# Optimization experiments

Measured on AMD Instinct MI355X. Metric: run time of the kernel, lower is better.

Reference implementation:

```python
import jax, jax.numpy as jnp
import numpy as np

B, U, H, M, D = 64, 1024, 16, 512, 4  # batch, units, numheads, memsize, depth
HS = U // H  # headsize


def setup_inputs() -> dict:
    key = jax.random.key(0)
    ks = jax.random.split(key, 6)
    scale = 0.02
    return {
        "x": jax.random.normal(ks[0], (B, U), jnp.float32),
        "memory": jax.random.normal(ks[1], (B, M * U), jnp.float32),
        "Wr": jax.random.normal(ks[2], (D, U, H * (M + 1)), jnp.float32) * scale,
        "br": jnp.zeros((D, H * (M + 1)), jnp.float32),
        "Ww": jax.random.normal(ks[3], (D, U, H * M), jnp.float32) * scale,
        "bw": jnp.zeros((D, H * M), jnp.float32),
        "Wk": jax.random.normal(ks[4], (D, U, U), jnp.float32) * scale,
        "bk": jnp.zeros((D, U), jnp.float32),
    }


def reference(x, memory, Wr, br, Ww, bw, Wk, bk):
    b = x.shape[0]
    mem4 = memory.reshape(b, M, H, HS)          # [B, M, H, HS]
    out = x
    for l in range(D):  # fixed small depth loop over structurally distinct layers
        inp4 = out.reshape(b, 1, H, HS)
        att = jnp.concatenate([mem4, inp4], axis=1)        # [B, M+1, H, HS]
        memstate = att.reshape(b, M + 1, U).mean(axis=1)   # [B, U]
        # read attention: per-head softmax over memory slots (+input slot)
        rlog = memstate @ Wr[l] + br[l]                    # [B, H*(M+1)]
        rw = jax.nn.softmax(rlog.reshape(b, M + 1, H), axis=1)  # [B, M+1, H]
        att = att * rw[..., None]                          # weighted read
        newval = jax.nn.relu(att.reshape(b, M + 1, U).sum(axis=1) @ Wk[l] + bk[l])  # [B, U]
        # write attention: per-head softmax over memory slots
        wlog = newval @ Ww[l] + bw[l]                      # [B, H*M]
        ww = jax.nn.softmax(wlog.reshape(b, M, H), axis=1)[..., None]  # [B, M, H, 1]
        mem4 = (1.0 - ww) * mem4 + ww * newval.reshape(b, 1, H, HS)
        out = newval
    return out, mem4.reshape(b, M * U)
```

## Files before the change

kernel.cpp:

```cpp
#include <hip/hip_runtime.h>

#define BB 64
#define UU 1024
#define HH 16
#define MM 512
#define DD 4
#define NR 8208
#define NW 8192
#define NK 1024

__device__ inline float warp_reduce_max(float v) {
    #pragma unroll
    for (int off = 32; off > 0; off >>= 1) v = fmaxf(v, __shfl_xor(v, off));
    return v;
}
__device__ inline float warp_reduce_sum(float v) {
    #pragma unroll
    for (int off = 32; off > 0; off >>= 1) v += __shfl_xor(v, off);
    return v;
}

__global__ void k_zero(float* __restrict__ p) {
    p[blockIdx.x * 256 + threadIdx.x] = 0.0f;
}

__global__ __launch_bounds__(256) void k_memsum(const float* __restrict__ mem,
                                                float* __restrict__ memsum) {
    const int b = blockIdx.x, mc = blockIdx.y, t = threadIdx.x;
    const float4* src = (const float4*)(mem + (size_t)b * MM * UU);
    float4 s = make_float4(0.f, 0.f, 0.f, 0.f);
    const int m0 = mc * 32;
    for (int m = m0; m < m0 + 32; ++m) {
        float4 v = src[(size_t)m * 256 + t];
        s.x += v.x; s.y += v.y; s.z += v.z; s.w += v.w;
    }
    float* d = memsum + b * UU + t * 4;
    atomicAdd(d + 0, s.x); atomicAdd(d + 1, s.y);
    atomicAdd(d + 2, s.z); atomicAdd(d + 3, s.w);
}

__global__ void k_prep_r(const float* __restrict__ memsum, const float* __restrict__ out,
                         float* __restrict__ memstate, float* __restrict__ wsum) {
    int i = blockIdx.x * 256 + threadIdx.x;
    memstate[i] = (memsum[i] + out[i]) * (1.0f / 513.0f);
    wsum[i] = 0.0f;
}

__global__ __launch_bounds__(256) void k_gemm(const float* __restrict__ A,
                                              const float* __restrict__ W,
                                              float* __restrict__ pbuf,
                                              int N, int kchunk, int kcl2 ) {
    __shared__ float At[256 * 64];
    const int t = threadIdx.x;
    const int cb = blockIdx.x * 128;
    const int ks = blockIdx.y;
    const int kbase = ks * kchunk;

    const int n4 = kchunk >> 4;
    const int kq_mask = (kchunk >> 2) - 1;
    for (int i = 0; i < n4; ++i) {
        int idx4 = t + (i << 8);
        int r = idx4 >> kcl2;
        int kq = idx4 & kq_mask;
        float4 v = *(const float4*)(A + r * UU + kbase + (kq << 2));
        int kk = kq << 2;
        At[(kk + 0) * 64 + r] = v.x;
        At[(kk + 1) * 64 + r] = v.y;
        At[(kk + 2) * 64 + r] = v.z;
        At[(kk + 3) * 64 + r] = v.w;
    }
    __syncthreads();

    const int wave = t >> 6;
    const int lane = t & 63;
    const int row0 = wave << 4;
    const int col = cb + (lane << 1);
    const bool wvalid = (col + 2 <= N);
    const float* Wp = W + (size_t)kbase * N + col;

    float acc[16][2];
    #pragma unroll
    for (int r = 0; r < 16; ++r) { acc[r][0] = 0.f; acc[r][1] = 0.f; }

    float2 wb0[8], wb1[8];
    if (wvalid) {
        #pragma unroll
        for (int i = 0; i < 8; ++i) wb0[i] = *(const float2*)(Wp + (size_t)i * N);
    }
    for (int kb = 0; kb < kchunk; kb += 8) {
        if (wvalid && (kb + 8 < kchunk)) {
            #pragma unroll
            for (int i = 0; i < 8; ++i)
                wb1[i] = *(const float2*)(Wp + (size_t)(kb + 8 + i) * N);
        }
        #pragma unroll
        for (int i = 0; i < 8; ++i) {
            const float* ap = &At[(kb + i) * 64 + row0];
            float a[16];
            *(float4*)&a[0]  = *(const float4*)(ap + 0);
            *(float4*)&a[4]  = *(const float4*)(ap + 4);
            *(float4*)&a[8]  = *(const float4*)(ap + 8);
            *(float4*)&a[12] = *(const float4*)(ap + 12);
            float2 wv = wb0[i];
            #pragma unroll
            for (int r = 0; r < 16; ++r) {
                acc[r][0] = fmaf(a[r], wv.x, acc[r][0]);
                acc[r][1] = fmaf(a[r], wv.y, acc[r][1]);
            }
        }
        #pragma unroll
        for (int i = 0; i < 8; ++i) wb0[i] = wb1[i];
    }

    if (wvalid) {
        float* dst = pbuf + (size_t)ks * 64 * N + col;
        #pragma unroll
        for (int r = 0; r < 16; ++r) {
            float2 o; o.x = acc[r][0]; o.y = acc[r][1];
            *(float2*)(dst + (size_t)(row0 + r) * N) = o;
        }
    }
}

__global__ __launch_bounds__(256) void k_softmax(const float* __restrict__ pbuf,
                                                 const float* __restrict__ bias,
                                                 float* __restrict__ outT,
                                                 int N, int S, int ksplit) {
    __shared__ float sm[4];
    const int b = blockIdx.x >> 4;
    const int h = blockIdx.x & 15;
    const int t = threadIdx.x;

    float v[3];
    float mx = -1e30f;
    #pragma unroll
    for (int i = 0; i < 3; ++i) {
        int slot = t + (i << 8);
        float val = -1e30f;
        if (slot < S) {
            int j = slot * HH + h;
            val = bias[j];
            for (int ks = 0; ks < ksplit; ++ks)
                val += pbuf[(size_t)(ks * BB + b) * N + j];
        }
        v[i] = val;
        mx = fmaxf(mx, val);
    }
    mx = warp_reduce_max(mx);
    if ((t & 63) == 0) sm[t >> 6] = mx;
    __syncthreads();
    mx = fmaxf(fmaxf(sm[0], sm[1]), fmaxf(sm[2], sm[3]));
    __syncthreads();

    float sum = 0.f;
    #pragma unroll
    for (int i = 0; i < 3; ++i) {
        int slot = t + (i << 8);
        if (slot < S) { v[i] = __expf(v[i] - mx); sum += v[i]; }
    }
    sum = warp_reduce_sum(sum);
    if ((t & 63) == 0) sm[t >> 6] = sum;
    __syncthreads();
    sum = sm[0] + sm[1] + sm[2] + sm[3];
    const float inv = 1.0f / sum;
    #pragma unroll
    for (int i = 0; i < 3; ++i) {
        int slot = t + (i << 8);
        if (slot < S) outT[(size_t)(b * HH + h) * S + slot] = v[i] * inv;
    }
}

__global__ __launch_bounds__(256) void k_passA(const float* __restrict__ mem,
                                               const float* __restrict__ rwT,
                                               float* __restrict__ wsum) {
    const int b = blockIdx.x, mc = blockIdx.y, t = threadIdx.x;
    const int h = t >> 4;
    const float4* src = (const float4*)(mem + (size_t)b * MM * UU);
    const float* rw = rwT + (size_t)(b * HH + h) * (MM + 1);
    float4 s = make_float4(0.f, 0.f, 0.f, 0.f);
    const int m0 = mc * 32;
    for (int m = m0; m < m0 + 32; ++m) {
        float wgt = rw[m];
        float4 v = src[(size_t)m * 256 + t];
        s.x = fmaf(wgt, v.x, s.x); s.y = fmaf(wgt, v.y, s.y);
        s.z = fmaf(wgt, v.z, s.z); s.w = fmaf(wgt, v.w, s.w);
    }
    float* d = wsum + b * UU + t * 4;
    atomicAdd(d + 0, s.x); atomicAdd(d + 1, s.y);
    atomicAdd(d + 2, s.z); atomicAdd(d + 3, s.w);
}

__global__ void k_prep_k(const float* __restrict__ wsum, const float* __restrict__ out,
                         const float* __restrict__ rwT, float* __restrict__ kin) {
    int i = blockIdx.x * 256 + threadIdx.x;
    int b = i >> 10, u = i & 1023;
    int h = u >> 6;
    float r = rwT[(size_t)(b * HH + h) * (MM + 1) + MM];
    kin[i] = fmaf(out[i], r, wsum[i]);
}

__global__ void k_relu(const float* __restrict__ pbuf, const float* __restrict__ bk,
                       float* __restrict__ newval, float* __restrict__ memsum,
                       float* __restrict__ outdst) {
    int i = blockIdx.x * 256 + threadIdx.x;
    int b = i >> 10, u = i & 1023;
    float v = bk[u];
    for (int ks = 0; ks < 32; ++ks) v += pbuf[(size_t)(ks * BB + b) * NK + u];
    v = fmaxf(v, 0.f);
    newval[i] = v;
    memsum[i] = 0.f;
    if (outdst) outdst[i] = v;
}

__global__ __launch_bounds__(256) void k_update(const float* __restrict__ src,
                                                float* __restrict__ dst,
                                                const float* __restrict__ wwT,
                                                const float* __restrict__ newval,
                                                float* __restrict__ memsum, int do_sum) {
    const int b = blockIdx.x, mc = blockIdx.y, t = threadIdx.x;
    const int h = t >> 4;
    const float4* s4 = (const float4*)(src + (size_t)b * MM * UU);
    float4* d4 = (float4*)(dst + (size_t)b * MM * UU);
    const float* ww = wwT + (size_t)(b * HH + h) * MM;
    float4 nv = *(const float4*)(newval + b * UU + t * 4);
    float4 acc = make_float4(0.f, 0.f, 0.f, 0.f);
    const int m0 = mc * 32;
    for (int m = m0; m < m0 + 32; ++m) {
        float wgt = ww[m];
        float4 v = s4[(size_t)m * 256 + t];
        v.x = fmaf(wgt, nv.x - v.x, v.x);
        v.y = fmaf(wgt, nv.y - v.y, v.y);
        v.z = fmaf(wgt, nv.z - v.z, v.z);
        v.w = fmaf(wgt, nv.w - v.w, v.w);
        d4[(size_t)m * 256 + t] = v;
        acc.x += v.x; acc.y += v.y; acc.z += v.z; acc.w += v.w;
    }
    if (do_sum) {
        float* d = memsum + b * UU + t * 4;
        atomicAdd(d + 0, acc.x); atomicAdd(d + 1, acc.y);
        atomicAdd(d + 2, acc.z); atomicAdd(d + 3, acc.w);
    }
}

extern "C" void kernel_launch(void* const* d_in, const int* in_sizes, int n_in,
                              void* d_out, int out_size, void* d_ws, size_t ws_size,
                              hipStream_t stream) {
    const float* x    = (const float*)d_in[0];
    const float* memI = (const float*)d_in[1];
    const float* Wr   = (const float*)d_in[2];
    const float* br   = (const float*)d_in[3];
    const float* Ww   = (const float*)d_in[4];
    const float* bw   = (const float*)d_in[5];
    const float* Wk   = (const float*)d_in[6];
    const float* bk   = (const float*)d_in[7];

    float* outp   = (float*)d_out;
    float* memOut = outp + BB * UU;

    char* w = (char*)d_ws;
    float* pbuf     = (float*)(w + 0);
    float* rwT      = (float*)(w + 8404992);
    float* wwT      = (float*)(w + 10506240);
    float* memsum   = (float*)(w + 12603392);
    float* wsum     = (float*)(w + 12865536);
    float* memstate = (float*)(w + 13127680);
    float* kin      = (float*)(w + 13389824);
    float* nv0      = (float*)(w + 13651968);
    float* nv1      = (float*)(w + 13914112);

    k_zero<<<BB * UU / 256, 256, 0, stream>>>(memsum);
    k_memsum<<<dim3(BB, 16), 256, 0, stream>>>(memI, memsum);

    const float* curOut = x;
    const float* curMem = memI;
    for (int l = 0; l < DD; ++l) {
        float* nv = (l & 1) ? nv1 : nv0;
        k_prep_r<<<BB * UU / 256, 256, 0, stream>>>(memsum, curOut, memstate, wsum);
        k_gemm<<<dim3(65, 4), 256, 0, stream>>>(memstate, Wr + (size_t)l * UU * NR, pbuf, NR, 256, 6);
        k_softmax<<<BB * HH, 256, 0, stream>>>(pbuf, br + (size_t)l * NR, rwT, NR, MM + 1, 4);
        k_passA<<<dim3(BB, 16), 256, 0, stream>>>(curMem, rwT, wsum);
        k_prep_k<<<BB * UU / 256, 256, 0, stream>>>(wsum, curOut, rwT, kin);
        k_gemm<<<dim3(8, 32), 256, 0, stream>>>(kin, Wk + (size_t)l * UU * NK, pbuf, NK, 32, 3);
        k_relu<<<BB * UU / 256, 256, 0, stream>>>(pbuf, bk + (size_t)l * NK, nv, memsum,
                                                  (l == DD - 1) ? outp : (float*)nullptr);
        k_gemm<<<dim3(64, 4), 256, 0, stream>>>(nv, Ww + (size_t)l * UU * NW, pbuf, NW, 256, 6);
        k_softmax<<<BB * HH, 256, 0, stream>>>(pbuf, bw + (size_t)l * NW, wwT, NW, MM, 4);
        k_update<<<dim3(BB, 16), 256, 0, stream>>>(curMem, memOut, wwT, nv, memsum,
                                                   (l < DD - 1) ? 1 : 0);
        curMem = memOut;
        curOut = nv;
    }
}
```

Baseline: 1.144 ms.

## Replace atomics with partial buffers, split GEMM K further, restructure softmax

```diff
diff --git a/kernel.cpp b/kernel.cpp
--- a/kernel.cpp
+++ b/kernel.cpp
@@ -9,48 +9,45 @@
 #define NW 8192
 #define NK 1024
 
-__device__ inline float warp_reduce_max(float v) {
+__device__ inline float wave_max(float v) {
     #pragma unroll
     for (int off = 32; off > 0; off >>= 1) v = fmaxf(v, __shfl_xor(v, off));
     return v;
 }
-__device__ inline float warp_reduce_sum(float v) {
+__device__ inline float wave_sum(float v) {
     #pragma unroll
     for (int off = 32; off > 0; off >>= 1) v += __shfl_xor(v, off);
     return v;
 }
 
-__global__ void k_zero(float* __restrict__ p) {
-    p[blockIdx.x * 256 + threadIdx.x] = 0.0f;
-}
-
 __global__ __launch_bounds__(256) void k_memsum(const float* __restrict__ mem,
-                                                float* __restrict__ memsum) {
+                                                float* __restrict__ msump) {
     const int b = blockIdx.x, mc = blockIdx.y, t = threadIdx.x;
     const float4* src = (const float4*)(mem + (size_t)b * MM * UU);
     float4 s = make_float4(0.f, 0.f, 0.f, 0.f);
     const int m0 = mc * 32;
+    #pragma unroll 8
     for (int m = m0; m < m0 + 32; ++m) {
         float4 v = src[(size_t)m * 256 + t];
         s.x += v.x; s.y += v.y; s.z += v.z; s.w += v.w;
     }
-    float* d = memsum + b * UU + t * 4;
-    atomicAdd(d + 0, s.x); atomicAdd(d + 1, s.y);
-    atomicAdd(d + 2, s.z); atomicAdd(d + 3, s.w);
-}
-
-__global__ void k_prep_r(const float* __restrict__ memsum, const float* __restrict__ out,
-                         float* __restrict__ memstate, float* __restrict__ wsum) {
+    *(float4*)(msump + (size_t)(mc * BB + b) * UU + t * 4) = s;
+}
+
+__global__ void k_prep_r(const float* __restrict__ msump, const float* __restrict__ out,
+                         float* __restrict__ memstate) {
     int i = blockIdx.x * 256 + threadIdx.x;
-    memstate[i] = (memsum[i] + out[i]) * (1.0f / 513.0f);
-    wsum[i] = 0.0f;
-}
-
-__global__ __launch_bounds__(256) void k_gemm(const float* __restrict__ A,
-                                              const float* __restrict__ W,
-                                              float* __restrict__ pbuf,
-                                              int N, int kchunk, int kcl2 ) {
-    __shared__ float At[256 * 64];
+    float s = out[i];
+    #pragma unroll
+    for (int mc = 0; mc < 16; ++mc) s += msump[i + mc * (BB * UU)];
+    memstate[i] = s * (1.0f / 513.0f);
+}
+
+__global__ __launch_bounds__(256, 2) void k_gemm(const float* __restrict__ A,
+                                                 const float* __restrict__ W,
+                                                 float* __restrict__ pbuf,
+                                                 int N, int kchunk, int kcl2) {
+    extern __shared__ float At[];
     const int t = threadIdx.x;
     const int cb = blockIdx.x * 128;
     const int ks = blockIdx.y;
@@ -122,93 +119,106 @@
     }
 }
 
-__global__ __launch_bounds__(256) void k_softmax(const float* __restrict__ pbuf,
-                                                 const float* __restrict__ bias,
-                                                 float* __restrict__ outT,
-                                                 int N, int S, int ksplit) {
-    __shared__ float sm[4];
-    const int b = blockIdx.x >> 4;
-    const int h = blockIdx.x & 15;
+__global__ __launch_bounds__(256) void k_redT(const float* __restrict__ pbuf,
+                                              const float* __restrict__ bias,
+                                              float* __restrict__ outT,
+                                              int N, int S, int ksplit) {
+    __shared__ float sm[256 * 17];
+    const int b = blockIdx.x;
+    const int j0 = blockIdx.y * 4096;
+    const int nj = min(4096, N - j0);
     const int t = threadIdx.x;
 
-    float v[3];
+    for (int o = t; o < nj; o += 256) {
+        int j = j0 + o;
+        float val = bias[j];
+        for (int ks = 0; ks < ksplit; ++ks)
+            val += pbuf[(size_t)(ks * BB + b) * N + j];
+        sm[(o >> 4) * 17 + (o & 15)] = val;
+    }
+    __syncthreads();
+
+    const int slot0 = j0 >> 4;
+    const int ns = nj >> 4;
+    if (ns == 256) {
+        #pragma unroll
+        for (int h = 0; h < 16; ++h)
+            outT[(size_t)(b * HH + h) * S + slot0 + t] = sm[t * 17 + h];
+    } else {
+        for (int idx = t; idx < nj; idx += 256) {
+            int h = idx / ns, s = idx - h * ns;
+            outT[(size_t)(b * HH + h) * S + slot0 + s] = sm[s * 17 + h];
+        }
+    }
+}
+
+__global__ __launch_bounds__(256) void k_softmax2(float* __restrict__ T, int S) {
+    const int row = blockIdx.x * 4 + (threadIdx.x >> 6);
+    const int lane = threadIdx.x & 63;
+    float* p = T + (size_t)row * S;
+    const int n = (S + 63) >> 6;
+    float v[9];
     float mx = -1e30f;
-    #pragma unroll
-    for (int i = 0; i < 3; ++i) {
-        int slot = t + (i << 8);
-        float val = -1e30f;
-        if (slot < S) {
-            int j = slot * HH + h;
-            val = bias[j];
-            for (int ks = 0; ks < ksplit; ++ks)
-                val += pbuf[(size_t)(ks * BB + b) * N + j];
-        }
+    for (int i = 0; i < n; ++i) {
+        int s = lane + (i << 6);
+        float val = (s < S) ? p[s] : -1e30f;
         v[i] = val;
         mx = fmaxf(mx, val);
     }
-    mx = warp_reduce_max(mx);
-    if ((t & 63) == 0) sm[t >> 6] = mx;
-    __syncthreads();
-    mx = fmaxf(fmaxf(sm[0], sm[1]), fmaxf(sm[2], sm[3]));
-    __syncthreads();
-
+    mx = wave_max(mx);
     float sum = 0.f;
-    #pragma unroll
-    for (int i = 0; i < 3; ++i) {
-        int slot = t + (i << 8);
-        if (slot < S) { v[i] = __expf(v[i] - mx); sum += v[i]; }
-    }
-    sum = warp_reduce_sum(sum);
-    if ((t & 63) == 0) sm[t >> 6] = sum;
-    __syncthreads();
-    sum = sm[0] + sm[1] + sm[2] + sm[3];
+    for (int i = 0; i < n; ++i) {
+        int s = lane + (i << 6);
+        if (s < S) { v[i] = __expf(v[i] - mx); sum += v[i]; }
+    }
+    sum = wave_sum(sum);
     const float inv = 1.0f / sum;
-    #pragma unroll
-    for (int i = 0; i < 3; ++i) {
-        int slot = t + (i << 8);
-        if (slot < S) outT[(size_t)(b * HH + h) * S + slot] = v[i] * inv;
+    for (int i = 0; i < n; ++i) {
+        int s = lane + (i << 6);
+        if (s < S) p[s] = v[i] * inv;
     }
 }
 
 __global__ __launch_bounds__(256) void k_passA(const float* __restrict__ mem,
                                                const float* __restrict__ rwT,
-                                               float* __restrict__ wsum) {
+                                               float* __restrict__ ppar) {
     const int b = blockIdx.x, mc = blockIdx.y, t = threadIdx.x;
     const int h = t >> 4;
     const float4* src = (const float4*)(mem + (size_t)b * MM * UU);
     const float* rw = rwT + (size_t)(b * HH + h) * (MM + 1);
     float4 s = make_float4(0.f, 0.f, 0.f, 0.f);
     const int m0 = mc * 32;
+    #pragma unroll 8
     for (int m = m0; m < m0 + 32; ++m) {
         float wgt = rw[m];
         float4 v = src[(size_t)m * 256 + t];
         s.x = fmaf(wgt, v.x, s.x); s.y = fmaf(wgt, v.y, s.y);
         s.z = fmaf(wgt, v.z, s.z); s.w = fmaf(wgt, v.w, s.w);
     }
-    float* d = wsum + b * UU + t * 4;
-    atomicAdd(d + 0, s.x); atomicAdd(d + 1, s.y);
-    atomicAdd(d + 2, s.z); atomicAdd(d + 3, s.w);
-}
-
-__global__ void k_prep_k(const float* __restrict__ wsum, const float* __restrict__ out,
+    *(float4*)(ppar + (size_t)(mc * BB + b) * UU + t * 4) = s;
+}
+
+__global__ void k_prep_k(const float* __restrict__ ppar, const float* __restrict__ out,
                          const float* __restrict__ rwT, float* __restrict__ kin) {
     int i = blockIdx.x * 256 + threadIdx.x;
     int b = i >> 10, u = i & 1023;
     int h = u >> 6;
+    float s = 0.f;
+    #pragma unroll
+    for (int mc = 0; mc < 16; ++mc) s += ppar[i + mc * (BB * UU)];
     float r = rwT[(size_t)(b * HH + h) * (MM + 1) + MM];
-    kin[i] = fmaf(out[i], r, wsum[i]);
+    kin[i] = fmaf(out[i], r, s);
 }
 
 __global__ void k_relu(const float* __restrict__ pbuf, const float* __restrict__ bk,
-                       float* __restrict__ newval, float* __restrict__ memsum,
-                       float* __restrict__ outdst) {
+                       float* __restrict__ newval, float* __restrict__ outdst) {
     int i = blockIdx.x * 256 + threadIdx.x;
-    int b = i >> 10, u = i & 1023;
+    int u = i & 1023;
     float v = bk[u];
-    for (int ks = 0; ks < 32; ++ks) v += pbuf[(size_t)(ks * BB + b) * NK + u];
+    #pragma unroll
+    for (int ks = 0; ks < 32; ++ks) v += pbuf[i + ks * (BB * UU)];
     v = fmaxf(v, 0.f);
     newval[i] = v;
-    memsum[i] = 0.f;
     if (outdst) outdst[i] = v;
 }
 
@@ -216,7 +226,7 @@
                                                 float* __restrict__ dst,
                                                 const float* __restrict__ wwT,
                                                 const float* __restrict__ newval,
-                                                float* __restrict__ memsum, int do_sum) {
+                                                float* __restrict__ msump, int do_sum) {
     const int b = blockIdx.x, mc = blockIdx.y, t = threadIdx.x;
     const int h = t >> 4;
     const float4* s4 = (const float4*)(src + (size_t)b * MM * UU);
@@ -225,6 +235,7 @@
     float4 nv = *(const float4*)(newval + b * UU + t * 4);
     float4 acc = make_float4(0.f, 0.f, 0.f, 0.f);
     const int m0 = mc * 32;
+    #pragma unroll 8
     for (int m = m0; m < m0 + 32; ++m) {
         float wgt = ww[m];
         float4 v = s4[(size_t)m * 256 + t];
@@ -235,11 +246,8 @@
         d4[(size_t)m * 256 + t] = v;
         acc.x += v.x; acc.y += v.y; acc.z += v.z; acc.w += v.w;
     }
-    if (do_sum) {
-        float* d = memsum + b * UU + t * 4;
-        atomicAdd(d + 0, acc.x); atomicAdd(d + 1, acc.y);
-        atomicAdd(d + 2, acc.z); atomicAdd(d + 3, acc.w);
-    }
+    if (do_sum)
+        *(float4*)(msump + (size_t)(mc * BB + b) * UU + t * 4) = acc;
 }
 
 extern "C" void kernel_launch(void* const* d_in, const int* in_sizes, int n_in,
@@ -259,33 +267,37 @@
 
     char* w = (char*)d_ws;
     float* pbuf     = (float*)(w + 0);
-    float* rwT      = (float*)(w + 8404992);
-    float* wwT      = (float*)(w + 10506240);
-    float* memsum   = (float*)(w + 12603392);
-    float* wsum     = (float*)(w + 12865536);
-    float* memstate = (float*)(w + 13127680);
-    float* kin      = (float*)(w + 13389824);
-    float* nv0      = (float*)(w + 13651968);
-    float* nv1      = (float*)(w + 13914112);
-
-    k_zero<<<BB * UU / 256, 256, 0, stream>>>(memsum);
-    k_memsum<<<dim3(BB, 16), 256, 0, stream>>>(memI, memsum);
+    float* ppar     = (float*)(w + 16809984);
+    float* msump    = (float*)(w + 21004288);
+    float* rwT      = (float*)(w + 25198592);
+    float* wwT      = (float*)(w + 27299840);
+    float* memstate = (float*)(w + 29396992);
+    float* kin      = (float*)(w + 29659136);
+    float* nv0      = (float*)(w + 29921280);
+    float* nv1      = (float*)(w + 30183424);
+
+    k_memsum<<<dim3(BB, 16), 256, 0, stream>>>(memI, msump);
 
     const float* curOut = x;
     const float* curMem = memI;
     for (int l = 0; l < DD; ++l) {
         float* nv = (l & 1) ? nv1 : nv0;
-        k_prep_r<<<BB * UU / 256, 256, 0, stream>>>(memsum, curOut, memstate, wsum);
-        k_gemm<<<dim3(65, 4), 256, 0, stream>>>(memstate, Wr + (size_t)l * UU * NR, pbuf, NR, 256, 6);
-        k_softmax<<<BB * HH, 256, 0, stream>>>(pbuf, br + (size_t)l * NR, rwT, NR, MM + 1, 4);
-        k_passA<<<dim3(BB, 16), 256, 0, stream>>>(curMem, rwT, wsum);
-        k_prep_k<<<BB * UU / 256, 256, 0, stream>>>(wsum, curOut, rwT, kin);
-        k_gemm<<<dim3(8, 32), 256, 0, stream>>>(kin, Wk + (size_t)l * UU * NK, pbuf, NK, 32, 3);
-        k_relu<<<BB * UU / 256, 256, 0, stream>>>(pbuf, bk + (size_t)l * NK, nv, memsum,
+        k_prep_r<<<BB * UU / 256, 256, 0, stream>>>(msump, curOut, memstate);
+        k_gemm<<<dim3(65, 8), 256, 128 * 64 * 4, stream>>>(
+            memstate, Wr + (size_t)l * UU * NR, pbuf, NR, 128, 5);
+        k_redT<<<dim3(BB, 3), 256, 0, stream>>>(pbuf, br + (size_t)l * NR, rwT, NR, MM + 1, 8);
+        k_softmax2<<<256, 256, 0, stream>>>(rwT, MM + 1);
+        k_passA<<<dim3(BB, 16), 256, 0, stream>>>(curMem, rwT, ppar);
+        k_prep_k<<<BB * UU / 256, 256, 0, stream>>>(ppar, curOut, rwT, kin);
+        k_gemm<<<dim3(8, 32), 256, 32 * 64 * 4, stream>>>(
+            kin, Wk + (size_t)l * UU * NK, pbuf, NK, 32, 3);
+        k_relu<<<BB * UU / 256, 256, 0, stream>>>(pbuf, bk + (size_t)l * NK, nv,
                                                   (l == DD - 1) ? outp : (float*)nullptr);
-        k_gemm<<<dim3(64, 4), 256, 0, stream>>>(nv, Ww + (size_t)l * UU * NW, pbuf, NW, 256, 6);
-        k_softmax<<<BB * HH, 256, 0, stream>>>(pbuf, bw + (size_t)l * NW, wwT, NW, MM, 4);
-        k_update<<<dim3(BB, 16), 256, 0, stream>>>(curMem, memOut, wwT, nv, memsum,
+        k_gemm<<<dim3(64, 8), 256, 128 * 64 * 4, stream>>>(
+            nv, Ww + (size_t)l * UU * NW, pbuf, NW, 128, 5);
+        k_redT<<<dim3(BB, 2), 256, 0, stream>>>(pbuf, bw + (size_t)l * NW, wwT, NW, MM, 8);
+        k_softmax2<<<256, 256, 0, stream>>>(wwT, MM);
+        k_update<<<dim3(BB, 16), 256, 0, stream>>>(curMem, memOut, wwT, nv, msump,
                                                    (l < DD - 1) ? 1 : 0);
         curMem = memOut;
         curOut = nv;
```

New measurement: 1.226 ms. +7.2%, slower.
